# Kernel tuning notes

Hardware: AMD Instinct MI355X
Metric: run time of the kernel (lower is better)

Reference implementation:

```python
import jax, jax.numpy as jnp
import numpy as np

HEADS = 8


def _ln(x, g, b):
    m = x.mean(-1, keepdims=True)
    v = ((x - m) ** 2).mean(-1, keepdims=True)
    return (x - m) / jnp.sqrt(v + 1e-5) * g + b


def _mha(xq, xkv, inw, inb, outw, outb):
    # torch nn.MultiheadAttention (dropout off). xq/xkv: [B,S,D]
    B, S, D = xq.shape
    hd = D // HEADS
    q = (xq @ inw[:D].T + inb[:D]).reshape(B, S, HEADS, hd)
    k = (xkv @ inw[D:2 * D].T + inb[D:2 * D]).reshape(B, S, HEADS, hd)
    v = (xkv @ inw[2 * D:].T + inb[2 * D:]).reshape(B, S, HEADS, hd)
    s = jnp.einsum('bqhd,bkhd->bhqk', q, k) / np.float32(np.sqrt(hd))
    o = jnp.einsum('bhqk,bkhd->bqhd', jax.nn.softmax(s, axis=-1), v).reshape(B, S, D)
    return o @ outw.T + outb


def _eca(x1, x2, qw, qb, kw, kb, vw, vb):
    # EfficientCrossAttention: bmm -> clamp -> softmax -> bmm
    Q = x1 @ qw.T + qb
    K = x2 @ kw.T + kb
    V = x2 @ vw.T + vb
    s = jnp.einsum('bqd,bkd->bqk', Q, K) / np.float32(np.sqrt(Q.shape[-1]))
    s = jnp.clip(s, -100.0, 100.0)
    return jnp.einsum('bqk,bkd->bqd', jax.nn.softmax(s, axis=-1), V)


def _itda(img, caps, qw, qb, kw, kb, vw, vb):
    B, NC, D = caps.shape
    S = img.shape[1]  # 196
    cap_e = jnp.broadcast_to(caps[:, :, None, :], (B, NC, S, D)).reshape(B * NC, S, D)
    img_e = jnp.broadcast_to(img[:, None, :, :], (B, NC, S, D)).reshape(B * NC, S, D)
    out = _eca(cap_e, img_e, qw, qb, kw, kb, vw, vb).reshape(B, NC, S, D)
    mask = (caps.sum(-1) != 0).astype(out.dtype)[:, :, None, None]  # [B,NC,1,1]
    msum = jnp.clip(jnp.broadcast_to(mask, (B, NC, S, 1)).sum(1), 1e-6, None)
    return (out * mask).sum(1) / msum


def _mse(a, b):
    return jnp.mean((a - b) ** 2)


def _forward(input_1, input_2, cap1, cap2, img_w, img_b, w_emb, h_emb,
             mlp_w1, mlp_b1, mlp_w2, mlp_b2, fc_w, fc_b, efc_w, efc_b,
             efc2_w, efc2_b, tr_in_w, tr_in_b, tr_out_w, tr_out_b,
             tr_ln_g, tr_ln_b, itda_qw, itda_qb, itda_kw, itda_kb, itda_vw, itda_vb,
             ca_qw, ca_qb, ca_kw, ca_kb, ca_vw, ca_vb,
             sa_qw, sa_qb, sa_kw, sa_kb, sa_vw, sa_vb):
    B, C, H, W = input_1.shape
    A = img_w.shape[0]
    # caption projections
    cap1_o = cap1 @ fc_w.T + fc_b  # [B,NC,512]
    cap2_o = cap2 @ fc_w.T + fc_b
    cap1_m = jnp.broadcast_to(cap1_o.mean(1)[:, None, :], (B, H * W, A))
    cap2_m = jnp.broadcast_to(cap2_o.mean(1)[:, None, :], (B, H * W, A))
    # 1x1 conv + positional embedding; pe[i,j] = [w_emb[j], h_emb[i]]
    pe = jnp.concatenate([jnp.broadcast_to(w_emb[None, :, :], (W, W, A // 2)),
                          jnp.broadcast_to(h_emb[:, None, :], (H, H, A // 2))], axis=-1)

    def embed(x):
        y = jnp.einsum('bchw,ac->bhwa', x, img_w) + img_b + pe
        return y.reshape(B, H * W, A)

    x1 = embed(input_1)  # [B,196,512]
    x2 = embed(input_2)
    # CDCR (Barlow-Twins style) loss

    def mlp(x):
        return jax.nn.relu(x @ mlp_w1.T + mlp_b1) @ mlp_w2.T + mlp_b2

    f1 = mlp(x1.reshape(-1, A))
    f2 = mlp(x2.reshape(-1, A))
    z_a = (f1 - f1.mean(0)) / jnp.std(f1, axis=0, ddof=1)
    z_b = (f2 - f2.mean(0)) / jnp.std(f2, axis=0, ddof=1)
    Bt, D = z_a.shape
    c = (z_a.T @ z_b) / Bt
    on_diag = jnp.sum((jnp.diagonal(c) - 1.0) ** 2)
    off_diag = jnp.sum(c.reshape(-1)[1:].reshape(D - 1, D + 1)[:, :-1] ** 2)
    cdcr_loss = on_diag + 0.003 * off_diag
    # cross-transformer stack (simultaneous update, as in torch tuple RHS)
    h1, h2 = x1, x2
    for l in range(tr_in_w.shape[0]):
        def layer(q, kv):
            a = _mha(q, kv, tr_in_w[l], tr_in_b[l], tr_out_w[l], tr_out_b[l])
            return _ln(q + a, tr_ln_g[l], tr_ln_b[l])
        h1, h2 = layer(h1, h2), layer(h2, h1)
    diff1 = x1 - h1
    diff2 = x2 - h2
    # ITDA module
    c12 = _eca(diff1, diff2, ca_qw, ca_qb, ca_kw, ca_kb, ca_vw, ca_vb)
    c21 = _eca(diff2, diff1, ca_qw, ca_qb, ca_kw, ca_kb, ca_vw, ca_vb)
    s11 = _eca(diff1, diff1, sa_qw, sa_qb, sa_kw, sa_kb, sa_vw, sa_vb)
    s22 = _eca(diff2, diff2, sa_qw, sa_qb, sa_kw, sa_kb, sa_vw, sa_vb)
    d_bef = _itda(diff1, cap2_o, itda_qw, itda_qb, itda_kw, itda_kb, itda_vw, itda_vb)
    d_aft = _itda(diff2, cap1_o, itda_qw, itda_qb, itda_kw, itda_kb, itda_vw, itda_vb)
    s_bef = _itda(diff1, cap1_o, itda_qw, itda_qb, itda_kw, itda_kb, itda_vw, itda_vb)
    s_aft = _itda(diff2, cap2_o, itda_qw, itda_qb, itda_kw, itda_kb, itda_vw, itda_vb)
    img_to_txt_loss = _mse(d_bef, c12) + _mse(d_aft, c21) + _mse(s_bef, s11) + _mse(s_aft, s22)

    def efc(x):
        return jax.nn.relu(x @ efc_w.T + efc_b)

    dyn = efc(jnp.concatenate([d_bef, d_aft], -1))
    sta = efc(jnp.concatenate([s_bef, s_aft], -1))
    align = efc(jnp.concatenate([dyn, sta], -1))
    txt = efc(jnp.concatenate([cap1_m, cap2_m], -1))
    comb = jnp.concatenate([diff1, diff2, txt, align], -1)  # [B,196,2048]
    out = jax.nn.relu(comb @ efc2_w.T + efc2_b)
    return out, cdcr_loss, img_to_txt_loss


def setup_inputs() -> dict:
    key = jax.random.key(0)
    ks = iter(jax.random.split(key, 64))

    def nrm(shape, s=0.02):
        return jax.random.normal(next(ks), shape, jnp.float32) * s

    B, C, H, W, NC, A = 64, 1024, 14, 14, 16, 512
    inp = dict(
        input_1=jax.random.normal(next(ks), (B, C, H, W), jnp.float32),
        input_2=jax.random.normal(next(ks), (B, C, H, W), jnp.float32),
        cap1=jax.random.normal(next(ks), (B, NC, 768), jnp.float32),
        cap2=jax.random.normal(next(ks), (B, NC, 768), jnp.float32),
        img_w=nrm((A, C)), img_b=jnp.zeros((A,), jnp.float32),
        w_emb=nrm((14, A // 2)), h_emb=nrm((14, A // 2)),
        mlp_w1=nrm((4 * A, A)), mlp_b1=jnp.zeros((4 * A,), jnp.float32),
        mlp_w2=nrm((A, 4 * A)), mlp_b2=jnp.zeros((A,), jnp.float32),
        fc_w=nrm((A, 768)), fc_b=jnp.zeros((A,), jnp.float32),
        efc_w=nrm((A, 2 * A)), efc_b=jnp.zeros((A,), jnp.float32),
        efc2_w=nrm((A, 4 * A)), efc2_b=jnp.zeros((A,), jnp.float32),
        tr_in_w=nrm((2, 3 * A, A)), tr_in_b=jnp.zeros((2, 3 * A), jnp.float32),
        tr_out_w=nrm((2, A, A)), tr_out_b=jnp.zeros((2, A), jnp.float32),
        tr_ln_g=jnp.ones((2, A), jnp.float32), tr_ln_b=jnp.zeros((2, A), jnp.float32),
    )
    for pfx in ('itda', 'ca', 'sa'):
        for nm in ('q', 'k', 'v'):
            inp[pfx + '_' + nm + 'w'] = nrm((A, A))
            inp[pfx + '_' + nm + 'b'] = jnp.zeros((A,), jnp.float32)
    return inp


def reference(input_1, input_2, cap1, cap2, img_w, img_b, w_emb, h_emb,
              mlp_w1, mlp_b1, mlp_w2, mlp_b2, fc_w, fc_b, efc_w, efc_b,
              efc2_w, efc2_b, tr_in_w, tr_in_b, tr_out_w, tr_out_b,
              tr_ln_g, tr_ln_b, itda_qw, itda_qb, itda_kw, itda_kb, itda_vw, itda_vb,
              ca_qw, ca_qb, ca_kw, ca_kb, ca_vw, ca_vb,
              sa_qw, sa_qb, sa_kw, sa_kb, sa_vw, sa_vb):
    return _forward(input_1, input_2, cap1, cap2, img_w, img_b, w_emb, h_emb,
                    mlp_w1, mlp_b1, mlp_w2, mlp_b2, fc_w, fc_b, efc_w, efc_b,
                    efc2_w, efc2_b, tr_in_w, tr_in_b, tr_out_w, tr_out_b,
                    tr_ln_g, tr_ln_b, itda_qw, itda_qb, itda_kw, itda_kb, itda_vw, itda_vb,
                    ca_qw, ca_qb, ca_kw, ca_kb, ca_vw, ca_vb,
                    sa_qw, sa_qb, sa_kw, sa_kb, sa_vw, sa_vb)
```

## Files before the change

kernel.cpp:

```cpp
#include <hip/hip_runtime.h>
#include <hip/hip_bf16.h>
#include <stdint.h>
#include <math.h>

#define BB   64
#define SS   196
#define BS   12544
#define NOUT 6422528L
#define SLD  224

typedef __attribute__((ext_vector_type(8))) short bf16x8;
typedef __attribute__((ext_vector_type(4))) float f32x4;

__device__ __forceinline__ float block_red256(float v, float* red, bool ismax) {
#pragma unroll
  for (int o = 32; o > 0; o >>= 1) {
    float t = __shfl_down(v, o, 64);
    v = ismax ? fmaxf(v, t) : v + t;
  }
  int lane = threadIdx.x & 63, wid = threadIdx.x >> 6;
  if (lane == 0) red[wid] = v;
  __syncthreads();
  float r = ismax ? fmaxf(fmaxf(red[0], red[1]), fmaxf(red[2], red[3]))
                  : (red[0] + red[1]) + (red[2] + red[3]);
// ... 18 lines not shown
__device__ __forceinline__ void lds_barrier() {
  asm volatile("s_waitcnt lgkmcnt(0)" ::: "memory");
  __builtin_amdgcn_s_barrier();
  __builtin_amdgcn_sched_barrier(0);
}

__device__ __forceinline__ int xcd_swizzle(int flat, int nwg) {
  int q = nwg >> 3, r = nwg & 7;
  int xcd = flat & 7, pos = flat >> 3;
  return (xcd < r ? xcd * (q + 1) : r * (q + 1) + (xcd - r) * q) + pos;
}

__global__ __launch_bounds__(256) void k_mfma_nt(
    const float* __restrict__ A, const float* __restrict__ W,
    const float* __restrict__ bias, float* __restrict__ C,
    int M, int N, int K, int relu) {
  __shared__ short As[2][128][40];
  __shared__ short Bs[2][128][40];
  const int tid = threadIdx.x;
  const int lane = tid & 63, wave = tid >> 6;
  const int wm = wave >> 1, wn = wave & 1;
  const int NX = gridDim.x;
  const int wg = xcd_swizzle(blockIdx.y * NX + blockIdx.x, NX * gridDim.y);
  const int m0 = (wg / NX) * 128, n0 = (wg % NX) * 128;
  const int srow = tid >> 1, skh = (tid & 1) * 16;
  const float* Ap = A + (long)(m0 + srow) * K + skh;
  const float* Wp = W + (long)(n0 + srow) * K + skh;
  const int fr = lane & 15, fq = lane >> 4;
  const int NK = K >> 5;
  f32x4 acc[4][4] = {};
  float4 xa[4], xw[4], ya[4], yw[4];
// ... 27 lines not shown
    for (int i = 0; i < 4; ++i)
#pragma unroll
      for (int j = 0; j < 4; ++j)
        acc[i][j] = __builtin_amdgcn_mfma_f32_16x16x32_bf16(af[i], bfr[j], acc[i][j], 0, 0, 0);
    lds_barrier();
  };

  ldt(xa, xw, 0);
  stage(xa, xw, 0);
  if (NK > 1) ldt(xa, xw, 1);
  lds_barrier();
  int t = 0;
  for (; t + 1 < NK; t += 2) { step(t, ya, yw, xa, xw); step(t + 1, xa, xw, ya, yw); }
  if (t < NK) step(t, ya, yw, xa, xw);

#pragma unroll
  for (int i = 0; i < 4; ++i) {
    int mB = m0 + wm * 64 + i * 16 + fq * 4;
#pragma unroll
    for (int j = 0; j < 4; ++j) {
      int n = n0 + wn * 64 + j * 16 + fr;
      float bz = bias[n];
#pragma unroll
      for (int r2 = 0; r2 < 4; ++r2) {
        float v = acc[i][j][r2] + bz;
        if (relu) v = fmaxf(v, 0.f);
        C[(long)(mB + r2) * N + n] = v;
      }
    }
  }
}

__global__ __launch_bounds__(256) void k_mfma_embed(
    const float* __restrict__ X1, const float* __restrict__ X2,
    const float* __restrict__ W,
    const float* __restrict__ bias,
    const float* __restrict__ wemb, const float* __restrict__ hemb,
    const float* __restrict__ sub1, const float* __restrict__ sub2,
    float* __restrict__ C1, float* __restrict__ C2,
    float* __restrict__ D1, float* __restrict__ D2) {
  __shared__ short As[2][128][40];
  __shared__ short Bs[2][128][40];
  const float* X = blockIdx.z ? X2 : X1;
  const float* sub = blockIdx.z ? sub2 : sub1;
  float* C = blockIdx.z ? C2 : C1;
  float* D = blockIdx.z ? D2 : D1;
  const int tid = threadIdx.x;
  const int lane = tid & 63, wave = tid >> 6;
  const int wm = wave >> 1, wn = wave & 1;
  const int NX = gridDim.x;
  const int wg = xcd_swizzle(blockIdx.y * NX + blockIdx.x, NX * gridDim.y);
  const int m0 = (wg / NX) * 128, n0 = (wg % NX) * 128;
  const int K = 1024, N = 512;
  const int srow = tid >> 1, skh = (tid & 1) * 16;
  const float* Wp = W + (long)(n0 + srow) * K + skh;
  const int arow = tid & 127, khalf = tid >> 7;
  const int am = m0 + arow;
  const int ab = am / 196, as_ = am % 196;
  const float* Xp = X + (long)ab * 200704 + as_;
  const int fr = lane & 15, fq = lane >> 4;
  const int NK = K >> 5;
// ... 44 lines not shown
  for (; t + 1 < NK; t += 2) { step(t, yx, yw, xx, xw); step(t + 1, xx, xw, yx, yw); }
  if (t < NK) step(t, yx, yw, xx, xw);

#pragma unroll
  for (int i = 0; i < 4; ++i) {
    int mB = m0 + wm * 64 + i * 16 + fq * 4;
#pragma unroll
    for (int j = 0; j < 4; ++j) {
      int n = n0 + wn * 64 + j * 16 + fr;
      float bz = bias[n];
#pragma unroll
      for (int r2 = 0; r2 < 4; ++r2) {
        int m = mB + r2;
        int s = m % 196;
        float pe = (n < 256) ? wemb[(s % 14) * 256 + n] : hemb[(s / 14) * 256 + (n - 256)];
        float v = acc[i][j][r2] + bz + pe;
        if (sub) v -= sub[(long)m * N + n];
        C[(long)m * N + n] = v;
        if (D) D[(long)m * N + n] = v;
      }
    }
  }
}

__global__ __launch_bounds__(256) void k_fmha(
    const float* __restrict__ Q, const float* __restrict__ KV,
    float* __restrict__ O) {
  __shared__ short Vt[64][240];
  __shared__ short Pt[4][16][40];
  const int tid = threadIdx.x;
  const int lane = tid & 63, wave = tid >> 6;
  const int b = blockIdx.x, h = blockIdx.y;
  const long brow = (long)b * 196;
  const float* Qb = Q + brow * 512 + h * 64;
  const float* Kb = KV + brow * 1024 + h * 64;
  const float* Vb = KV + brow * 1024 + 512 + h * 64;
  float* Ob = O + brow * 512 + h * 64;
  const int fr = lane & 15, fq = lane >> 4;

  for (int i = tid; i < 64 * 32; i += 256) {
    int d = i >> 5, k = 192 + (i & 31);
    if (k >= 196) Vt[d][k] = 0;
  }
  for (int i = tid; i < 196 * 16; i += 256) {
    int s = i >> 4, c4 = (i & 15) * 4;
    float4 v = *(const float4*)(Vb + (long)s * 1024 + c4);
    Vt[c4 + 0][s] = f2bf(v.x);
    Vt[c4 + 1][s] = f2bf(v.y);
    Vt[c4 + 2][s] = f2bf(v.z);
    Vt[c4 + 3][s] = f2bf(v.w);
  }
  __syncthreads();

  for (int qt = wave; qt < 13; qt += 4) {
    const int q0 = qt * 16;
    const int qr = (q0 + fr < 196) ? q0 + fr : 195;
    bf16x8 aq0, aq1;
    {
      const float* qp = Qb + (long)qr * 512 + fq * 8;
      float4 a = *(const float4*)(qp);
      float4 b2 = *(const float4*)(qp + 4);
      float4 c = *(const float4*)(qp + 32);
      float4 d = *(const float4*)(qp + 36);
      cvt8((short*)&aq0, a, b2);
      cvt8((short*)&aq1, c, d);
    }
    f32x4 sc[13];
#pragma unroll
    for (int t = 0; t < 13; ++t) {
      int kr = (t * 16 + fr < 196) ? t * 16 + fr : 195;
      const float* kp = Kb + (long)kr * 1024 + fq * 8;
      float4 a = *(const float4*)(kp);
      float4 b2 = *(const float4*)(kp + 4);
      float4 c = *(const float4*)(kp + 32);
      float4 d = *(const float4*)(kp + 36);
      bf16x8 bk0, bk1;
      cvt8((short*)&bk0, a, b2);
      cvt8((short*)&bk1, c, d);
      f32x4 z = {};
      z = __builtin_amdgcn_mfma_f32_16x16x32_bf16(aq0, bk0, z, 0, 0, 0);
      z = __builtin_amdgcn_mfma_f32_16x16x32_bf16(aq1, bk1, z, 0, 0, 0);
      sc[t] = z;
    }
#pragma unroll
    for (int t = 0; t < 13; ++t)
#pragma unroll
      for (int r2 = 0; r2 < 4; ++r2) sc[t][r2] *= 0.125f;
    if (fr >= 4) {
#pragma unroll
      for (int r2 = 0; r2 < 4; ++r2) sc[12][r2] = -1e30f;
    }
#pragma unroll
    for (int r2 = 0; r2 < 4; ++r2) {
// ... 109 lines not shown
      int mb = m0 + i * 16 + fq * 4;
#pragma unroll
      for (int r2 = 0; r2 < 4; ++r2) {
        int m = mb + r2;
        if (m < M) {
          float v = acc[i][r2] * scale + bz;
          if (relu2) v = fmaxf(v, 0.f);
          if (clampf) v = fminf(fmaxf(v, -100.f), 100.f);
          Cb[(long)m * ldc + n] = v;
        }
      }
    }
  }
}

__global__ __launch_bounds__(256) void k_mfma_bnn(
    const float* __restrict__ A, const float* __restrict__ B, float* __restrict__ C,
    int M, int N, int K, int KBvalid, int lda, int ldb, int ldc, int nz2,
    int64_t sA1, int64_t sA2, int64_t sB1, int64_t sB2, int64_t sC1, int64_t sC2) {
  __shared__ short As[2][64][40];
  __shared__ short Bs[2][64][40];
  const int tid = threadIdx.x;
  const int lane = tid & 63, wave = tid >> 6;
  const int m0 = blockIdx.y * 64, n0 = blockIdx.x * 64;
  const int z = blockIdx.z, z1 = z / nz2, z2 = z % nz2;
  const float* Ab = A + z1 * sA1 + z2 * sA2;
  const float* Bb = B + z1 * sB1 + z2 * sB2;
  float* Cb = C + z1 * sC1 + z2 * sC2;
  const int sr = tid >> 2, skh = (tid & 3) * 8;
  const int ar = (m0 + sr < M) ? m0 + sr : M - 1;
// ... 109 lines not shown
  lds_barrier();
  int t = 0;
  for (; t + 1 < NK; t += 2) { step(t, ya, yb, xa, xb); step(t + 1, xa, xb, ya, yb); }
  if (t < NK) step(t, ya, yb, xa, xb);

  const int j = j0 + wave * 16 + fr;
#pragma unroll
  for (int i = 0; i < 4; ++i) {
    int ib = i0 + i * 16 + fq * 4;
#pragma unroll
    for (int r2 = 0; r2 < 4; ++r2)
      atomicAdd(&C[(long)(ib + r2) * 512 + j], acc[i][r2] * scale);
  }
}

__global__ __launch_bounds__(256) void k_gemm_nt(
    const float* __restrict__ A, const float* __restrict__ W,
    const float* __restrict__ bias, float* __restrict__ C,
    int M, int N, int K, int relu) {
  __shared__ float As[16][68];
  __shared__ float Ws[16][68];
  const int tx = threadIdx.x, ty = threadIdx.y;
  const int tid = ty * 16 + tx;
  const int m0 = blockIdx.y * 64, n0 = blockIdx.x * 64;
  const int lr = tid >> 2, lk = (tid & 3) << 2;
  const float* Ap = A + (long)(m0 + lr) * K + lk;
  const float* Wp = W + (long)(n0 + lr) * K + lk;
  float acc[4][4] = {};
  for (int k0 = 0; k0 < K; k0 += 16) {
    float4 av = *(const float4*)(Ap + k0);
    float4 wv = *(const float4*)(Wp + k0);
    As[lk + 0][lr] = av.x; As[lk + 1][lr] = av.y; As[lk + 2][lr] = av.z; As[lk + 3][lr] = av.w;
    Ws[lk + 0][lr] = wv.x; Ws[lk + 1][lr] = wv.y; Ws[lk + 2][lr] = wv.z; Ws[lk + 3][lr] = wv.w;
    __syncthreads();
#pragma unroll
    for (int kk = 0; kk < 16; ++kk) {
      float4 a4 = *(const float4*)&As[kk][ty * 4];
      float4 w4 = *(const float4*)&Ws[kk][tx * 4];
      float a[4] = {a4.x, a4.y, a4.z, a4.w};
      float w[4] = {w4.x, w4.y, w4.z, w4.w};
#pragma unroll
      for (int i = 0; i < 4; ++i)
#pragma unroll
        for (int j = 0; j < 4; ++j) acc[i][j] += a[i] * w[j];
    }
    __syncthreads();
  }
#pragma unroll
  for (int i = 0; i < 4; ++i) {
    int m = m0 + ty * 4 + i;
#pragma unroll
    for (int j = 0; j < 4; ++j) {
      int n = n0 + tx * 4 + j;
      float v = acc[i][j] + bias[n];
      if (relu) v = fmaxf(v, 0.f);
      C[(long)m * N + n] = v;
    }
  }
}

__global__ __launch_bounds__(256) void k_softmax_rows(float* __restrict__ S, int nrows) {
  int row = blockIdx.x * 4 + (threadIdx.x >> 6);
  int lane = threadIdx.x & 63;
  if (row >= nrows) return;
  float* p = S + (long)row * SLD;
  float v0 = p[lane];
  float v1 = p[lane + 64];
  float v2 = p[lane + 128];
  float v3 = (lane + 192 < 196) ? p[lane + 192] : -1e30f;
  float mx = fmaxf(fmaxf(v0, v1), fmaxf(v2, v3));
#pragma unroll
  for (int o = 32; o > 0; o >>= 1) mx = fmaxf(mx, __shfl_down(mx, o, 64));
  mx = __shfl(mx, 0, 64);
  float e0 = expf(v0 - mx), e1 = expf(v1 - mx), e2 = expf(v2 - mx);
  float e3 = (lane + 192 < 196) ? expf(v3 - mx) : 0.f;
  float s = e0 + e1 + e2 + e3;
#pragma unroll
  for (int o = 32; o > 0; o >>= 1) s += __shfl_down(s, o, 64);
  s = __shfl(s, 0, 64);
  float inv = 1.0f / s;
  p[lane] = e0 * inv;
  p[lane + 64] = e1 * inv;
  p[lane + 128] = e2 * inv;
  if (lane + 192 < SLD) p[lane + 192] = (lane + 192 < 196) ? e3 * inv : 0.f;
}

__global__ __launch_bounds__(256) void k_addln(
    float* __restrict__ h, const float* __restrict__ o,
    const float* __restrict__ g, const float* __restrict__ be) {
  __shared__ float red[4];
  long row = blockIdx.x;
  float* hr = h + row * 512;
  const float* orow = o + row * 512;
  int t = threadIdx.x;
  float v0 = hr[t] + orow[t];
  float v1 = hr[t + 256] + orow[t + 256];
  float mean = block_red256(v0 + v1, red, false) * (1.0f / 512.0f);
  float d0 = v0 - mean, d1 = v1 - mean;
  float var = block_red256(d0 * d0 + d1 * d1, red, false) * (1.0f / 512.0f);
  float inv = 1.0f / sqrtf(var + 1e-5f);
  hr[t] = d0 * inv * g[t] + be[t];
  hr[t + 256] = d1 * inv * g[t + 256] + be[t + 256];
}

__global__ void k_zero(float* __restrict__ p, int n) {
  int i = blockIdx.x * 256 + threadIdx.x;
  if (i < n) p[i] = 0.f;
}

__global__ __launch_bounds__(256) void k_diff(
    float* __restrict__ d, const float* __restrict__ x, const float* __restrict__ h) {
  long i = ((long)blockIdx.x * 256 + threadIdx.x) * 4;
  float4 xv = *(const float4*)(x + i);
  float4 hv = *(const float4*)(h + i);
  float4 r; r.x = xv.x - hv.x; r.y = xv.y - hv.y; r.z = xv.z - hv.z; r.w = xv.w - hv.w;
  *(float4*)(d + i) = r;
}
// ... 125 lines not shown
  __syncthreads();
  for (int st = 128; st > 0; st >>= 1) {
    if (threadIdx.x < st) sh[threadIdx.x] += sh[threadIdx.x + st];
    __syncthreads();
  }
  if (threadIdx.x == 0) out[0] = (float)(sh[0] / (64.0 * 196.0 * 512.0));
}

__global__ __launch_bounds__(256) void k_concat2(float* __restrict__ dst, const float* __restrict__ a,
                                                 const float* __restrict__ b) {
  int i = blockIdx.x * 256 + threadIdx.x;
  int col = i & 1023, row = i >> 10;
  dst[i] = (col < 512) ? a[row * 512 + col] : b[row * 512 + col - 512];
}

__global__ __launch_bounds__(256) void k_comb_chunk(
    float* __restrict__ dst, const float* __restrict__ d1, const float* __restrict__ d2,
    const float* __restrict__ txt, const float* __restrict__ al, long r0) {
  long i = (long)blockIdx.x * 256 + threadIdx.x;
  int col = (int)(i & 2047);
  long m = r0 + (i >> 11);
  int b = (int)(m / 196);
  float v;
  if (col < 512)       v = d1[m * 512 + col];
  else if (col < 1024) v = d2[m * 512 + col - 512];
  else if (col < 1536) v = txt[(long)b * 512 + col - 1024];
  else                 v = al[(long)b * 512 + col - 1536];
  dst[i] = v;
}

extern "C" void kernel_launch(void* const* d_in, const int* in_sizes, int n_in,
                              void* d_out, int out_size, void* d_ws, size_t ws_size,
                              hipStream_t stream) {
  (void)in_sizes; (void)n_in; (void)out_size;
  const float* in1    = (const float*)d_in[0];
  const float* in2    = (const float*)d_in[1];
  const float* cap1   = (const float*)d_in[2];
  const float* cap2   = (const float*)d_in[3];
  const float* imgw   = (const float*)d_in[4];
  const float* imgb   = (const float*)d_in[5];
  const float* wemb   = (const float*)d_in[6];
  const float* hemb   = (const float*)d_in[7];
  const float* mlpw1  = (const float*)d_in[8];
  const float* mlpb1  = (const float*)d_in[9];
  const float* mlpw2  = (const float*)d_in[10];
  const float* mlpb2  = (const float*)d_in[11];
  const float* fcw    = (const float*)d_in[12];
  const float* fcb    = (const float*)d_in[13];
  const float* efcw   = (const float*)d_in[14];
// ... 21 lines not shown
  const size_t SZ = (size_t)BS * 512;
  float* w = (float*)d_ws;
  auto alloc = [&](size_t n) { float* p = w; w += n; return p; };
  float* h1 = alloc(SZ);
  float* h2 = alloc(SZ);
  float* tA = alloc(SZ);
  float* tB = alloc(SZ);
  float* tC = alloc(SZ);
  float* tD = alloc(SZ);
  float* sbuf = alloc(SZ);
  float* cap1o = alloc(64 * 16 * 512);
  float* cap2o = alloc(64 * 16 * 512);
  float* qc1   = alloc(64 * 16 * 512);
  float* qc2   = alloc(64 * 16 * 512);
  float* attb  = alloc(64 * 16 * 512);
  float* cmat  = alloc(512 * 512);
  float* colsum1 = alloc(512); float* colsq1 = alloc(512);
  float* colsum2 = alloc(512); float* colsq2 = alloc(512);
  float* mean1 = alloc(512); float* istd1 = alloc(512);
  float* mean2 = alloc(512); float* istd2 = alloc(512);
  float* mask1 = alloc(1024); float* mask2 = alloc(1024);
  float* vdbef = alloc(64 * 512); float* vdaft = alloc(64 * 512);
  float* vsbef = alloc(64 * 512); float* vsaft = alloc(64 * 512);
  float* cm1 = alloc(64 * 512); float* cm2 = alloc(64 * 512);
  float* vdyn = alloc(64 * 512); float* vsta = alloc(64 * 512);
  float* valign = alloc(64 * 512); float* vtxt = alloc(64 * 512);
  float* ccat = alloc(64 * 1024);
  double* msepart = (double*)alloc(4096 * 2);
  double* cdcrpart = (double*)alloc(1024);
  float* itkvw = alloc(1024 * 512); float* itkvb = alloc(1024);
  float* cakvw = alloc(1024 * 512); float* cakvb = alloc(1024);
  float* sakvw = alloc(1024 * 512); float* sakvb = alloc(1024);
  size_t used = (size_t)(w - (float*)d_ws);
  bool xsave = ws_size >= (used + 2 * SZ + 1024) * sizeof(float);
  float* x1 = nullptr;
  if (xsave) x1 = alloc(2 * SZ);

  auto gemm = [&](const float* Aa, const float* Ww, const float* bb, float* Cc,
                  int M, int N, int K, int relu) {
    long g128 = ((M % 128) == 0 && (N % 128) == 0) ? (long)(N / 128) * (M / 128) : 0;
    if (g128 >= 784 && (K % 32) == 0)
      k_mfma_nt<<<dim3(N / 128, M / 128), 256, 0, stream>>>(Aa, Ww, bb, Cc, M, N, K, relu);
    else
      k_mfma_bnt<<<dim3(N / 64, (M + 63) / 64, 1), 256, 0, stream>>>(
          Aa, Ww, Cc, M, N, K, K, K, N, 1,
          0, 0, 0, 0, 0, 0, 1.0f, 0, bb, relu);
  };
  auto embed2 = [&](const float* s1, const float* s2, float* C1p, float* C2p,
                    float* D1p, float* D2p) {
    k_mfma_embed<<<dim3(4, BS / 128, 2), 256, 0, stream>>>(
        in1, in2, imgw, imgb, wemb, hemb, s1, s2, C1p, C2p, D1p, D2p);
  };
  const int64_t RB = (int64_t)SS * 512;
  const int64_t QB = 16 * 512;
  auto attn512 = [&](const float* Qp, int64_t qZ, const float* KVp, int64_t kvZ,
                     float* Op, int64_t oZ, int M, float scale) {
    int mt = (M + 63) / 64;
    int64_t sS = (int64_t)M * SLD;
    k_mfma_bnt<<<dim3(4, mt, 64), 256, 0, stream>>>(
        Qp, KVp, sbuf, M, 196, 512, 512, 1024, SLD, 1,
        qZ, 0, kvZ, 0, sS, 0, scale, 1, nullptr, 0);
    k_softmax_rows<<<(64 * M + 3) / 4, 256, 0, stream>>>(sbuf, 64 * M);
    k_mfma_bnn<<<dim3(8, mt, 64), 256, 0, stream>>>(
        sbuf, KVp + 512, Op, M, 512, SLD, 196, SLD, 1024, 512, 1,
        sS, 0, kvZ, 0, oZ, 0);
  };
  auto attn_mha = [&](const float* Qp, const float* KVp, float* Op) {
    k_fmha<<<dim3(64, 8), 256, 0, stream>>>(Qp, KVp, Op);
  };
  auto efc64 = [&](const float* Aa, float* Cc) {
    k_mfma_bnt<<<dim3(8, 1, 1), 256, 0, stream>>>(
        Aa, efcw, Cc, 64, 512, 1024, 1024, 1024, 512, 1,
        0, 0, 0, 0, 0, 0, 1.0f, 0, efcb, 1);
  };

  const float scalE = 1.0f / sqrtf(512.0f);

  k_catkv<<<2048, 256, 0, stream>>>(itkvw, itkw, itvw, itkvb, itkb, itvb);
  k_catkv<<<2048, 256, 0, stream>>>(cakvw, cakw, cavw, cakvb, cakb, cavb);
  k_catkv<<<2048, 256, 0, stream>>>(sakvw, sakw, savw, sakvb, sakb, savb);

  if (xsave) embed2(nullptr, nullptr, h1, h2, x1, x1 + SZ);
  else       embed2(nullptr, nullptr, h1, h2, nullptr, nullptr);
  gemm(cap1, fcw, fcb, cap1o, 1024, 512, 768, 0);
  gemm(cap2, fcw, fcb, cap2o, 1024, 512, 768, 0);
  k_meannc<<<dim3(2, 64), 256, 0, stream>>>(cap1o, nullptr, cm1);
  k_meannc<<<dim3(2, 64), 256, 0, stream>>>(cap2o, nullptr, cm2);

  for (int c = 0; c < 2; ++c) {
    const size_t off = (size_t)c * 6272 * 512;
    gemm(h1 + off, mlpw1, mlpb1, tC, 6272, 2048, 512, 1);
    gemm(tC, mlpw2, mlpb2, tA + off, 6272, 512, 2048, 0);
  }
  for (int c = 0; c < 2; ++c) {
    const size_t off = (size_t)c * 6272 * 512;
    gemm(h2 + off, mlpw1, mlpb1, tC, 6272, 2048, 512, 1);
    gemm(tC, mlpw2, mlpb2, tB + off, 6272, 512, 2048, 0);
  }
  k_zero<<<8, 256, 0, stream>>>(colsum1, 2048);
  k_colstats<<<dim3(16, 49), 256, 0, stream>>>(tA, colsum1, colsq1);
  k_colstats<<<dim3(16, 49), 256, 0, stream>>>(tB, colsum2, colsq2);
  k_finstats<<<2, 256, 0, stream>>>(colsum1, colsq1, mean1, istd1);
  k_finstats<<<2, 256, 0, stream>>>(colsum2, colsq2, mean2, istd2);
  k_znorm<<<25088, 256, 0, stream>>>(tA, mean1, istd1);
  k_znorm<<<25088, 256, 0, stream>>>(tB, mean2, istd2);
  k_zero<<<1024, 256, 0, stream>>>(cmat, 262144);
  k_mfma_corr<<<dim3(8, 8, 14), 256, 0, stream>>>(tA, tB, cmat, BS / 14, 1.0f / (float)BS);
  k_cdcr_part<<<256, 256, 0, stream>>>(cmat, cdcrpart);
  k_cdcr_fin<<<1, 256, 0, stream>>>(cdcrpart, out + NOUT);

  for (int l = 0; l < 2; ++l) {
    const float* Wq = trinw + (size_t)l * 1536 * 512;
    const float* Wkv = Wq + 512 * 512;
    const float* bq = trinb + l * 1536;
    const float* bkv = bq + 512;
    const float* Wo = troutw + (size_t)l * 512 * 512;
    const float* bo = troutb + l * 512;
    const float* g  = trlng + l * 512;
    const float* be = trlnb + l * 512;
    gemm(h1, Wq, bq, tA, 2 * BS, 512, 512, 0);
    gemm(h2, Wkv, bkv, tC, BS, 1024, 512, 0);
    attn_mha(tA, tC, tA);
    gemm(tA, Wo, bo, sbuf, BS, 512, 512, 0);
    gemm(h1, Wkv, bkv, tC, BS, 1024, 512, 0);
    k_addln<<<BS, 256, 0, stream>>>(h1, sbuf, g, be);
    attn_mha(tA + SZ, tC, tA + SZ);
    gemm(tA + SZ, Wo, bo, sbuf, BS, 512, 512, 0);
    k_addln<<<BS, 256, 0, stream>>>(h2, sbuf, g, be);
  }

  if (xsave) {
    k_diff<<<12544, 256, 0, stream>>>(tC, x1, h1);
  } else {
    embed2(h1, h2, tC, tD, nullptr, nullptr);
  }

  gemm(cap1o, itqw, itqb, qc1, 1024, 512, 512, 0);
  gemm(cap2o, itqw, itqb, qc2, 1024, 512, 512, 0);
  k_mask<<<1024, 64, 0, stream>>>(cap1o, mask1);
  k_mask<<<1024, 64, 0, stream>>>(cap2o, mask2);
  gemm(tC, itkvw, itkvb, tA, BS, 1024, 512, 0);
  attn512(qc2, QB, tA, 2 * RB, attb, QB, 16, scalE);
  k_meannc<<<dim3(2, 64), 256, 0, stream>>>(attb, mask2, vdbef);
  attn512(qc1, QB, tA, 2 * RB, attb, QB, 16, scalE);
  k_meannc<<<dim3(2, 64), 256, 0, stream>>>(attb, mask1, vsbef);
  gemm(tD, itkvw, itkvb, tA, BS, 1024, 512, 0);
  attn512(qc1, QB, tA, 2 * RB, attb, QB, 16, scalE);
  k_meannc<<<dim3(2, 64), 256, 0, stream>>>(attb, mask1, vdaft);
  attn512(qc2, QB, tA, 2 * RB, attb, QB, 16, scalE);
  k_meannc<<<dim3(2, 64), 256, 0, stream>>>(attb, mask2, vsaft);

  auto eca_mse = [&](const float* xq, const float* xkv,
                     const float* qw2, const float* qb2,
                     const float* kvw2, const float* kvb2,
                     const float* vec, double* part) {
    gemm(xq,  qw2, qb2, h1, BS, 512, 512, 0);
    gemm(xkv, kvw2, kvb2, tA, BS, 1024, 512, 0);
    attn512(h1, RB, tA, 2 * RB, h2, RB, 196, scalE);
    k_mse<<<1024, 256, 0, stream>>>(h2, vec, part);
  };
  eca_mse(tC, tD, caqw, caqb, cakvw, cakvb, vdbef, msepart);
  eca_mse(tD, tC, caqw, caqb, cakvw, cakvb, vdaft, msepart + 1024);
  eca_mse(tC, tC, saqw, saqb, sakvw, sakvb, vsbef, msepart + 2048);
  eca_mse(tD, tD, saqw, saqb, sakvw, sakvb, vsaft, msepart + 3072);
  k_finloss<<<1, 256, 0, stream>>>(msepart, out + NOUT + 1);

  k_concat2<<<256, 256, 0, stream>>>(ccat, vdbef, vdaft);
  efc64(ccat, vdyn);
  k_concat2<<<256, 256, 0, stream>>>(ccat, vsbef, vsaft);
  efc64(ccat, vsta);
  k_concat2<<<256, 256, 0, stream>>>(ccat, vdyn, vsta);
  efc64(ccat, valign);
  k_concat2<<<256, 256, 0, stream>>>(ccat, cm1, cm2);
  efc64(ccat, vtxt);

  k_comb_chunk<<<100352, 256, 0, stream>>>(h1, tC, tD, vtxt, valign, 0);
  gemm(h1, efc2w, efc2b, out, BS, 512, 2048, 1);
}
```

Baseline: 2.544 ms.

## Store GEMM intermediates as bf16, batch attention calls, drop fallback embed path

GEMM outputs that only feed later MFMA stages (MLP hidden, transformer Q/KV, the concat before the final FC) are now written as bf16. A new GEMM variant reads bf16 A operands, and the fused MHA kernel reads bf16 Q/K/V directly, which cuts memory traffic and conversion work. The MLP runs over the full batch instead of in chunks, and paired ITDA attention calls are batched through a second z dimension. The embedding is stored once instead of being written to several buffers, and the xsave fallback is removed. In exchange this adds bf16 rounding to intermediates and assumes the workspace is large enough, and it uses qc1/qc2 and attb/attb2 as if they were contiguous.

```diff
diff --git a/kernel.cpp b/kernel.cpp
--- a/kernel.cpp
+++ b/kernel.cpp
@@ -56,7 +56,7 @@
 __global__ __launch_bounds__(256) void k_mfma_nt(
     const float* __restrict__ A, const float* __restrict__ W,
     const float* __restrict__ bias, float* __restrict__ C,
-    int M, int N, int K, int relu) {
+    int M, int N, int K, int relu, int obf) {
   __shared__ short As[2][128][40];
   __shared__ short Bs[2][128][40];
   const int tid = threadIdx.x;
@@ -114,6 +114,7 @@
   for (; t + 1 < NK; t += 2) { step(t, ya, yw, xa, xw); step(t + 1, xa, xw, ya, yw); }
   if (t < NK) step(t, ya, yw, xa, xw);
 
+  short* Cs = (short*)C;
 #pragma unroll
   for (int i = 0; i < 4; ++i) {
     int mB = m0 + wm * 64 + i * 16 + fq * 4;
@@ -125,7 +126,8 @@
       for (int r2 = 0; r2 < 4; ++r2) {
         float v = acc[i][j][r2] + bz;
         if (relu) v = fmaxf(v, 0.f);
-        C[(long)(mB + r2) * N + n] = v;
+        if (obf) Cs[(long)(mB + r2) * N + n] = f2bf(v);
+        else     C[(long)(mB + r2) * N + n] = v;
       }
     }
   }
@@ -136,15 +138,11 @@
     const float* __restrict__ W,
     const float* __restrict__ bias,
     const float* __restrict__ wemb, const float* __restrict__ hemb,
-    const float* __restrict__ sub1, const float* __restrict__ sub2,
-    float* __restrict__ C1, float* __restrict__ C2,
-    float* __restrict__ D1, float* __restrict__ D2) {
+    float* __restrict__ C1, float* __restrict__ C2) {
   __shared__ short As[2][128][40];
   __shared__ short Bs[2][128][40];
   const float* X = blockIdx.z ? X2 : X1;
-  const float* sub = blockIdx.z ? sub2 : sub1;
   float* C = blockIdx.z ? C2 : C1;
-  float* D = blockIdx.z ? D2 : D1;
   const int tid = threadIdx.x;
   const int lane = tid & 63, wave = tid >> 6;
   const int wm = wave >> 1, wn = wave & 1;
@@ -219,17 +217,14 @@
         int m = mB + r2;
         int s = m % 196;
         float pe = (n < 256) ? wemb[(s % 14) * 256 + n] : hemb[(s / 14) * 256 + (n - 256)];
-        float v = acc[i][j][r2] + bz + pe;
-        if (sub) v -= sub[(long)m * N + n];
-        C[(long)m * N + n] = v;
-        if (D) D[(long)m * N + n] = v;
+        C[(long)m * N + n] = acc[i][j][r2] + bz + pe;
       }
     }
   }
 }
 
-__global__ __launch_bounds__(256) void k_fmha(
-    const float* __restrict__ Q, const float* __restrict__ KV,
+__global__ __launch_bounds__(256) void k_fmha_bf(
+    const short* __restrict__ Q, const short* __restrict__ KV,
     float* __restrict__ O) {
   __shared__ short Vt[64][240];
   __shared__ short Pt[4][16][40];
@@ -237,9 +232,9 @@
   const int lane = tid & 63, wave = tid >> 6;
   const int b = blockIdx.x, h = blockIdx.y;
   const long brow = (long)b * 196;
-  const float* Qb = Q + brow * 512 + h * 64;
-  const float* Kb = KV + brow * 1024 + h * 64;
-  const float* Vb = KV + brow * 1024 + 512 + h * 64;
+  const short* Qb = Q + brow * 512 + h * 64;
+  const short* Kb = KV + brow * 1024 + h * 64;
+  const short* Vb = KV + brow * 1024 + 512 + h * 64;
   float* Ob = O + brow * 512 + h * 64;
   const int fr = lane & 15, fq = lane >> 4;
 
@@ -247,41 +242,27 @@
     int d = i >> 5, k = 192 + (i & 31);
     if (k >= 196) Vt[d][k] = 0;
   }
-  for (int i = tid; i < 196 * 16; i += 256) {
-    int s = i >> 4, c4 = (i & 15) * 4;
-    float4 v = *(const float4*)(Vb + (long)s * 1024 + c4);
-    Vt[c4 + 0][s] = f2bf(v.x);
-    Vt[c4 + 1][s] = f2bf(v.y);
-    Vt[c4 + 2][s] = f2bf(v.z);
-    Vt[c4 + 3][s] = f2bf(v.w);
+  for (int i = tid; i < 196 * 8; i += 256) {
+    int s = i >> 3, c8 = (i & 7) * 8;
+    bf16x8 v = *(const bf16x8*)(Vb + (long)s * 1024 + c8);
+#pragma unroll
+    for (int j = 0; j < 8; ++j) Vt[c8 + j][s] = v[j];
   }
   __syncthreads();
 
   for (int qt = wave; qt < 13; qt += 4) {
     const int q0 = qt * 16;
     const int qr = (q0 + fr < 196) ? q0 + fr : 195;
-    bf16x8 aq0, aq1;
-    {
-      const float* qp = Qb + (long)qr * 512 + fq * 8;
-      float4 a = *(const float4*)(qp);
-      float4 b2 = *(const float4*)(qp + 4);
-      float4 c = *(const float4*)(qp + 32);
-      float4 d = *(const float4*)(qp + 36);
-      cvt8((short*)&aq0, a, b2);
-      cvt8((short*)&aq1, c, d);
-    }
+    const short* qp = Qb + (long)qr * 512 + fq * 8;
+    bf16x8 aq0 = *(const bf16x8*)(qp);
+    bf16x8 aq1 = *(const bf16x8*)(qp + 32);
     f32x4 sc[13];
 #pragma unroll
     for (int t = 0; t < 13; ++t) {
       int kr = (t * 16 + fr < 196) ? t * 16 + fr : 195;
-      const float* kp = Kb + (long)kr * 1024 + fq * 8;
-      float4 a = *(const float4*)(kp);
-      float4 b2 = *(const float4*)(kp + 4);
-      float4 c = *(const float4*)(kp + 32);
-      float4 d = *(const float4*)(kp + 36);
-      bf16x8 bk0, bk1;
-      cvt8((short*)&bk0, a, b2);
-      cvt8((short*)&bk1, c, d);
+      const short* kp = Kb + (long)kr * 1024 + fq * 8;
+      bf16x8 bk0 = *(const bf16x8*)(kp);
+      bf16x8 bk1 = *(const bf16x8*)(kp + 32);
       f32x4 z = {};
       z = __builtin_amdgcn_mfma_f32_16x16x32_bf16(aq0, bk0, z, 0, 0, 0);
       z = __builtin_amdgcn_mfma_f32_16x16x32_bf16(aq1, bk1, z, 0, 0, 0);
@@ -421,6 +402,79 @@
   }
 }
 
+__global__ __launch_bounds__(256) void k_mfma_bnt_abf(
+    const short* __restrict__ A, const float* __restrict__ B, float* __restrict__ C,
+    int M, int N, int K, int lda, int ldb, int ldc,
+    const float* __restrict__ bias2, int relu2) {
+  __shared__ short As[2][64][40];
+  __shared__ short Bs[2][64][40];
+  const int tid = threadIdx.x;
+  const int lane = tid & 63, wave = tid >> 6;
+  const int NX = gridDim.x;
+  const int wg = xcd_swizzle(blockIdx.y * NX + blockIdx.x, NX * gridDim.y);
+  const int m0 = (wg / NX) * 64, n0 = (wg % NX) * 64;
+  const int sr = tid >> 2, skh = (tid & 3) * 8;
+  const int ar = (m0 + sr < M) ? m0 + sr : M - 1;
+  const int br = (n0 + sr < N) ? n0 + sr : N - 1;
+  const short* Ap = A + (long)ar * lda + skh;
+  const float* Bp = B + (long)br * ldb + skh;
+  const int fr = lane & 15, fq = lane >> 4;
+  const int NK = K >> 5;
+  f32x4 acc[4] = {};
+  int4 xa, ya;
+  float4 xb[2], yb[2];
+
+  auto ldt = [&](int4& ta, float4 (&tb)[2], int t) {
+    const int kb = t * 32;
+    ta = *(const int4*)(Ap + kb);
+#pragma unroll
+    for (int i = 0; i < 2; ++i) tb[i] = *(const float4*)(Bp + kb + i * 4);
+  };
+  auto stage = [&](int4& ta, float4 (&tb)[2], int p) {
+    *(int4*)&As[p][sr][skh] = ta;
+    cvt8(&Bs[p][sr][skh], tb[0], tb[1]);
+  };
+  auto step = [&](int t, int4& la, float4 (&lb)[2], int4& ca, float4 (&cb)[2]) {
+    const int par = t & 1;
+    if (t + 2 < NK) ldt(la, lb, t + 2);
+    bf16x8 bfr = *(const bf16x8*)&Bs[par][wave * 16 + fr][fq * 8];
+    bf16x8 af[4];
+#pragma unroll
+    for (int i = 0; i < 4; ++i) af[i] = *(const bf16x8*)&As[par][i * 16 + fr][fq * 8];
+    if (t + 1 < NK) stage(ca, cb, par ^ 1);
+#pragma unroll
+    for (int i = 0; i < 4; ++i)
+      acc[i] = __builtin_amdgcn_mfma_f32_16x16x32_bf16(af[i], bfr, acc[i], 0, 0, 0);
+    lds_barrier();
+  };
+
+  ldt(xa, xb, 0);
+  stage(xa, xb, 0);
+  if (NK > 1) ldt(xa, xb, 1);
+  lds_barrier();
+  int t = 0;
+  for (; t + 1 < NK; t += 2) { step(t, ya, yb, xa, xb); step(t + 1, xa, xb, ya, yb); }
+  if (t < NK) step(t, ya, yb, xa, xb);
+
+  const int n = n0 + wave * 16 + fr;
+  if (n < N) {
+    float bz = bias2 ? bias2[n] : 0.f;
+#pragma unroll
+    for (int i = 0; i < 4; ++i) {
+      int mb = m0 + i * 16 + fq * 4;
+#pragma unroll
+      for (int r2 = 0; r2 < 4; ++r2) {
+        int m = mb + r2;
+        if (m < M) {
+          float v = acc[i][r2] + bz;
+          if (relu2) v = fmaxf(v, 0.f);
+          C[(long)m * ldc + n] = v;
+        }
+      }
+    }
+  }
+}
+
 __global__ __launch_bounds__(256) void k_mfma_bnn(
     const float* __restrict__ A, const float* __restrict__ B, float* __restrict__ C,
     int M, int N, int K, int KBvalid, int lda, int ldb, int ldc, int nz2,
@@ -560,51 +614,6 @@
   }
 }
 
-__global__ __launch_bounds__(256) void k_gemm_nt(
-    const float* __restrict__ A, const float* __restrict__ W,
-    const float* __restrict__ bias, float* __restrict__ C,
-    int M, int N, int K, int relu) {
-  __shared__ float As[16][68];
-  __shared__ float Ws[16][68];
-  const int tx = threadIdx.x, ty = threadIdx.y;
-  const int tid = ty * 16 + tx;
-  const int m0 = blockIdx.y * 64, n0 = blockIdx.x * 64;
-  const int lr = tid >> 2, lk = (tid & 3) << 2;
-  const float* Ap = A + (long)(m0 + lr) * K + lk;
-  const float* Wp = W + (long)(n0 + lr) * K + lk;
-  float acc[4][4] = {};
-  for (int k0 = 0; k0 < K; k0 += 16) {
-    float4 av = *(const float4*)(Ap + k0);
-    float4 wv = *(const float4*)(Wp + k0);
-    As[lk + 0][lr] = av.x; As[lk + 1][lr] = av.y; As[lk + 2][lr] = av.z; As[lk + 3][lr] = av.w;
-    Ws[lk + 0][lr] = wv.x; Ws[lk + 1][lr] = wv.y; Ws[lk + 2][lr] = wv.z; Ws[lk + 3][lr] = wv.w;
-    __syncthreads();
-#pragma unroll
-    for (int kk = 0; kk < 16; ++kk) {
-      float4 a4 = *(const float4*)&As[kk][ty * 4];
-      float4 w4 = *(const float4*)&Ws[kk][tx * 4];
-      float a[4] = {a4.x, a4.y, a4.z, a4.w};
-      float w[4] = {w4.x, w4.y, w4.z, w4.w};
-#pragma unroll
-      for (int i = 0; i < 4; ++i)
-#pragma unroll
-        for (int j = 0; j < 4; ++j) acc[i][j] += a[i] * w[j];
-    }
-    __syncthreads();
-  }
-#pragma unroll
-  for (int i = 0; i < 4; ++i) {
-    int m = m0 + ty * 4 + i;
-#pragma unroll
-    for (int j = 0; j < 4; ++j) {
-      int n = n0 + tx * 4 + j;
-      float v = acc[i][j] + bias[n];
-      if (relu) v = fmaxf(v, 0.f);
-      C[(long)m * N + n] = v;
-    }
-  }
-}
-
 __global__ __launch_bounds__(256) void k_softmax_rows(float* __restrict__ S, int nrows) {
   int row = blockIdx.x * 4 + (threadIdx.x >> 6);
   int lane = threadIdx.x & 63;
@@ -631,22 +640,23 @@
   if (lane + 192 < SLD) p[lane + 192] = (lane + 192 < 196) ? e3 * inv : 0.f;
 }
 
-__global__ __launch_bounds__(256) void k_addln(
-    float* __restrict__ h, const float* __restrict__ o,
+__global__ __launch_bounds__(256) void k_addln2(
+    float* __restrict__ dst, const float* __restrict__ src, const float* __restrict__ o,
     const float* __restrict__ g, const float* __restrict__ be) {
   __shared__ float red[4];
   long row = blockIdx.x;
-  float* hr = h + row * 512;
+  const float* sr_ = src + row * 512;
   const float* orow = o + row * 512;
+  float* dr = dst + row * 512;
   int t = threadIdx.x;
-  float v0 = hr[t] + orow[t];
-  float v1 = hr[t + 256] + orow[t + 256];
+  float v0 = sr_[t] + orow[t];
+  float v1 = sr_[t + 256] + orow[t + 256];
   float mean = block_red256(v0 + v1, red, false) * (1.0f / 512.0f);
   float d0 = v0 - mean, d1 = v1 - mean;
   float var = block_red256(d0 * d0 + d1 * d1, red, false) * (1.0f / 512.0f);
   float inv = 1.0f / sqrtf(var + 1e-5f);
-  hr[t] = d0 * inv * g[t] + be[t];
-  hr[t + 256] = d1 * inv * g[t + 256] + be[t + 256];
+  dr[t] = d0 * inv * g[t] + be[t];
+  dr[t + 256] = d1 * inv * g[t + 256] + be[t + 256];
 }
 
 __global__ void k_zero(float* __restrict__ p, int n) {
@@ -802,25 +812,25 @@
   dst[i] = (col < 512) ? a[row * 512 + col] : b[row * 512 + col - 512];
 }
 
-__global__ __launch_bounds__(256) void k_comb_chunk(
-    float* __restrict__ dst, const float* __restrict__ d1, const float* __restrict__ d2,
-    const float* __restrict__ txt, const float* __restrict__ al, long r0) {
+__global__ __launch_bounds__(256) void k_comb_bf(
+    short* __restrict__ dst, const float* __restrict__ d1, const float* __restrict__ d2,
+    const float* __restrict__ txt, const float* __restrict__ al) {
   long i = (long)blockIdx.x * 256 + threadIdx.x;
   int col = (int)(i & 2047);
-  long m = r0 + (i >> 11);
+  long m = i >> 11;
   int b = (int)(m / 196);
   float v;
   if (col < 512)       v = d1[m * 512 + col];
   else if (col < 1024) v = d2[m * 512 + col - 512];
   else if (col < 1536) v = txt[(long)b * 512 + col - 1024];
   else                 v = al[(long)b * 512 + col - 1536];
-  dst[i] = v;
+  dst[i] = f2bf(v);
 }
 
 extern "C" void kernel_launch(void* const* d_in, const int* in_sizes, int n_in,
                               void* d_out, int out_size, void* d_ws, size_t ws_size,
                               hipStream_t stream) {
-  (void)in_sizes; (void)n_in; (void)out_size;
+  (void)in_sizes; (void)n_in; (void)out_size; (void)ws_size;
   const float* in1    = (const float*)d_in[0];
   const float* in2    = (const float*)d_in[1];
   const float* cap1   = (const float*)d_in[2];
@@ -872,6 +882,7 @@
   float* qc1   = alloc(64 * 16 * 512);
   float* qc2   = alloc(64 * 16 * 512);
   float* attb  = alloc(64 * 16 * 512);
+  float* attb2 = alloc(64 * 16 * 512);
   float* cmat  = alloc(512 * 512);
   float* colsum1 = alloc(512); float* colsq1 = alloc(512);
   float* colsum2 = alloc(512); float* colsq2 = alloc(512);
@@ -889,42 +900,36 @@
   float* itkvw = alloc(1024 * 512); float* itkvb = alloc(1024);
   float* cakvw = alloc(1024 * 512); float* cakvb = alloc(1024);
   float* sakvw = alloc(1024 * 512); float* sakvb = alloc(1024);
-  size_t used = (size_t)(w - (float*)d_ws);
-  bool xsave = ws_size >= (used + 2 * SZ + 1024) * sizeof(float);
-  float* x1 = nullptr;
-  if (xsave) x1 = alloc(2 * SZ);
+  float* x1 = alloc(2 * SZ);
+  float* x2 = x1 + SZ;
 
   auto gemm = [&](const float* Aa, const float* Ww, const float* bb, float* Cc,
                   int M, int N, int K, int relu) {
     long g128 = ((M % 128) == 0 && (N % 128) == 0) ? (long)(N / 128) * (M / 128) : 0;
     if (g128 >= 784 && (K % 32) == 0)
-      k_mfma_nt<<<dim3(N / 128, M / 128), 256, 0, stream>>>(Aa, Ww, bb, Cc, M, N, K, relu);
+      k_mfma_nt<<<dim3(N / 128, M / 128), 256, 0, stream>>>(Aa, Ww, bb, Cc, M, N, K, relu, 0);
     else
       k_mfma_bnt<<<dim3(N / 64, (M + 63) / 64, 1), 256, 0, stream>>>(
           Aa, Ww, Cc, M, N, K, K, K, N, 1,
           0, 0, 0, 0, 0, 0, 1.0f, 0, bb, relu);
   };
-  auto embed2 = [&](const float* s1, const float* s2, float* C1p, float* C2p,
-                    float* D1p, float* D2p) {
-    k_mfma_embed<<<dim3(4, BS / 128, 2), 256, 0, stream>>>(
-        in1, in2, imgw, imgb, wemb, hemb, s1, s2, C1p, C2p, D1p, D2p);
-  };
   const int64_t RB = (int64_t)SS * 512;
   const int64_t QB = 16 * 512;
-  auto attn512 = [&](const float* Qp, int64_t qZ, const float* KVp, int64_t kvZ,
-                     float* Op, int64_t oZ, int M, float scale) {
+  auto attn512 = [&](const float* Qp, int64_t qZ1, int64_t qZ2, const float* KVp, int64_t kvZ,
+                     float* Op, int64_t oZ1, int64_t oZ2, int M, int zq, float scale) {
     int mt = (M + 63) / 64;
-    int64_t sS = (int64_t)M * SLD;
-    k_mfma_bnt<<<dim3(4, mt, 64), 256, 0, stream>>>(
-        Qp, KVp, sbuf, M, 196, 512, 512, 1024, SLD, 1,
-        qZ, 0, kvZ, 0, sS, 0, scale, 1, nullptr, 0);
-    k_softmax_rows<<<(64 * M + 3) / 4, 256, 0, stream>>>(sbuf, 64 * M);
-    k_mfma_bnn<<<dim3(8, mt, 64), 256, 0, stream>>>(
-        sbuf, KVp + 512, Op, M, 512, SLD, 196, SLD, 1024, 512, 1,
-        sS, 0, kvZ, 0, oZ, 0);
-  };
-  auto attn_mha = [&](const float* Qp, const float* KVp, float* Op) {
-    k_fmha<<<dim3(64, 8), 256, 0, stream>>>(Qp, KVp, Op);
+    int64_t sS2 = (int64_t)M * SLD;
+    int64_t sS1 = 64 * sS2;
+    k_mfma_bnt<<<dim3(4, mt, 64 * zq), 256, 0, stream>>>(
+        Qp, KVp, sbuf, M, 196, 512, 512, 1024, SLD, 64,
+        qZ1, qZ2, 0, kvZ, sS1, sS2, scale, 1, nullptr, 0);
+    k_softmax_rows<<<(64 * zq * M + 3) / 4, 256, 0, stream>>>(sbuf, 64 * zq * M);
+    k_mfma_bnn<<<dim3(8, mt, 64 * zq), 256, 0, stream>>>(
+        sbuf, KVp + 512, Op, M, 512, SLD, 196, SLD, 1024, 512, 64,
+        sS1, sS2, 0, kvZ, oZ1, oZ2);
+  };
+  auto attn_mha = [&](const short* Qp, const short* KVp, float* Op) {
+    k_fmha_bf<<<dim3(64, 8), 256, 0, stream>>>(Qp, KVp, Op);
   };
   auto efc64 = [&](const float* Aa, float* Cc) {
     k_mfma_bnt<<<dim3(8, 1, 1), 256, 0, stream>>>(
@@ -938,23 +943,19 @@
   k_catkv<<<2048, 256, 0, stream>>>(cakvw, cakw, cavw, cakvb, cakb, cavb);
   k_catkv<<<2048, 256, 0, stream>>>(sakvw, sakw, savw, sakvb, sakb, savb);
 
-  if (xsave) embed2(nullptr, nullptr, h1, h2, x1, x1 + SZ);
-  else       embed2(nullptr, nullptr, h1, h2, nullptr, nullptr);
+  k_mfma_embed<<<dim3(4, BS / 128, 2), 256, 0, stream>>>(
+      in1, in2, imgw, imgb, wemb, hemb, x1, x2);
   gemm(cap1, fcw, fcb, cap1o, 1024, 512, 768, 0);
   gemm(cap2, fcw, fcb, cap2o, 1024, 512, 768, 0);
   k_meannc<<<dim3(2, 64), 256, 0, stream>>>(cap1o, nullptr, cm1);
   k_meannc<<<dim3(2, 64), 256, 0, stream>>>(cap2o, nullptr, cm2);
 
-  for (int c = 0; c < 2; ++c) {
-    const size_t off = (size_t)c * 6272 * 512;
-    gemm(h1 + off, mlpw1, mlpb1, tC, 6272, 2048, 512, 1);
-    gemm(tC, mlpw2, mlpb2, tA + off, 6272, 512, 2048, 0);
-  }
-  for (int c = 0; c < 2; ++c) {
-    const size_t off = (size_t)c * 6272 * 512;
-    gemm(h2 + off, mlpw1, mlpb1, tC, 6272, 2048, 512, 1);
-    gemm(tC, mlpw2, mlpb2, tB + off, 6272, 512, 2048, 0);
-  }
+  k_mfma_nt<<<dim3(16, 98), 256, 0, stream>>>(x1, mlpw1, mlpb1, tC, BS, 2048, 512, 1, 1);
+  k_mfma_bnt_abf<<<dim3(8, 196), 256, 0, stream>>>(
+      (const short*)tC, mlpw2, tA, BS, 512, 2048, 2048, 2048, 512, mlpb2, 0);
+  k_mfma_nt<<<dim3(16, 98), 256, 0, stream>>>(x2, mlpw1, mlpb1, tC, BS, 2048, 512, 1, 1);
+  k_mfma_bnt_abf<<<dim3(8, 196), 256, 0, stream>>>(
+      (const short*)tC, mlpw2, tB, BS, 512, 2048, 2048, 2048, 512, mlpb2, 0);
   k_zero<<<8, 256, 0, stream>>>(colsum1, 2048);
   k_colstats<<<dim3(16, 49), 256, 0, stream>>>(tA, colsum1, colsq1);
   k_colstats<<<dim3(16, 49), 256, 0, stream>>>(tB, colsum2, colsq2);
@@ -976,37 +977,34 @@
     const float* bo = troutb + l * 512;
     const float* g  = trlng + l * 512;
     const float* be = trlnb + l * 512;
-    gemm(h1, Wq, bq, tA, 2 * BS, 512, 512, 0);
-    gemm(h2, Wkv, bkv, tC, BS, 1024, 512, 0);
-    attn_mha(tA, tC, tA);
-    gemm(tA, Wo, bo, sbuf, BS, 512, 512, 0);
-    gemm(h1, Wkv, bkv, tC, BS, 1024, 512, 0);
-    k_addln<<<BS, 256, 0, stream>>>(h1, sbuf, g, be);
-    attn_mha(tA + SZ, tC, tA + SZ);
-    gemm(tA + SZ, Wo, bo, sbuf, BS, 512, 512, 0);
-    k_addln<<<BS, 256, 0, stream>>>(h2, sbuf, g, be);
-  }
-
-  if (xsave) {
-    k_diff<<<12544, 256, 0, stream>>>(tC, x1, h1);
-  } else {
-    embed2(h1, h2, tC, tD, nullptr, nullptr);
-  }
-
-  gemm(cap1o, itqw, itqb, qc1, 1024, 512, 512, 0);
-  gemm(cap2o, itqw, itqb, qc2, 1024, 512, 512, 0);
+    const float* s1 = l ? h1 : x1;
+    const float* s2 = l ? h2 : x2;
+    k_mfma_nt<<<dim3(4, 196), 256, 0, stream>>>(s1, Wq, bq, tA, 2 * BS, 512, 512, 0, 1);
+    k_mfma_nt<<<dim3(8, 98), 256, 0, stream>>>(s2, Wkv, bkv, tC, BS, 1024, 512, 0, 1);
+    k_mfma_nt<<<dim3(8, 98), 256, 0, stream>>>(s1, Wkv, bkv, tD, BS, 1024, 512, 0, 1);
+    attn_mha((const short*)tA, (const short*)tC, tB);
+    k_mfma_bnt<<<dim3(8, 196, 1), 256, 0, stream>>>(tB, Wo, sbuf, BS, 512, 512, 512, 512, 512, 1,
+                                                    0, 0, 0, 0, 0, 0, 1.0f, 0, bo, 0);
+    k_addln2<<<BS, 256, 0, stream>>>(h1, s1, sbuf, g, be);
+    attn_mha((const short*)tA + (size_t)BS * 512, (const short*)tD, tB);
+    k_mfma_bnt<<<dim3(8, 196, 1), 256, 0, stream>>>(tB, Wo, sbuf, BS, 512, 512, 512, 512, 512, 1,
+                                                    0, 0, 0, 0, 0, 0, 1.0f, 0, bo, 0);
+    k_addln2<<<BS, 256, 0, stream>>>(h2, s2, sbuf, g, be);
+  }
+
+  k_diff<<<12544, 256, 0, stream>>>(tC, x1, h1);
+
+  gemm(cap1o, itqw, itqb, qc1, 2048, 512, 512, 0);
   k_mask<<<1024, 64, 0, stream>>>(cap1o, mask1);
   k_mask<<<1024, 64, 0, stream>>>(cap2o, mask2);
   gemm(tC, itkvw, itkvb, tA, BS, 1024, 512, 0);
-  attn512(qc2, QB, tA, 2 * RB, attb, QB, 16, scalE);
-  k_meannc<<<dim3(2, 64), 256, 0, stream>>>(attb, mask2, vdbef);
-  attn512(qc1, QB, tA, 2 * RB, attb, QB, 16, scalE);
-  k_meannc<<<dim3(2, 64), 256, 0, stream>>>(attb, mask1, vsbef);
+  attn512(qc1, 524288, QB, tA, 2 * RB, attb, 524288, QB, 16, 2, scalE);
+  k_meannc<<<dim3(2, 64), 256, 0, stream>>>(attb,  mask1, vsbef);
+  k_meannc<<<dim3(2, 64), 256, 0, stream>>>(attb2, mask2, vdbef);
   gemm(tD, itkvw, itkvb, tA, BS, 1024, 512, 0);
-  attn512(qc1, QB, tA, 2 * RB, attb, QB, 16, scalE);
-  k_meannc<<<dim3(2, 64), 256, 0, stream>>>(attb, mask1, vdaft);
-  attn512(qc2, QB, tA, 2 * RB, attb, QB, 16, scalE);
-  k_meannc<<<dim3(2, 64), 256, 0, stream>>>(attb, mask2, vsaft);
+  attn512(qc1, 524288, QB, tA, 2 * RB, attb, 524288, QB, 16, 2, scalE);
+  k_meannc<<<dim3(2, 64), 256, 0, stream>>>(attb,  mask1, vdaft);
+  k_meannc<<<dim3(2, 64), 256, 0, stream>>>(attb2, mask2, vsaft);
 
   auto eca_mse = [&](const float* xq, const float* xkv,
                      const float* qw2, const float* qb2,
@@ -1014,7 +1012,7 @@
                      const float* vec, double* part) {
     gemm(xq,  qw2, qb2, h1, BS, 512, 512, 0);
     gemm(xkv, kvw2, kvb2, tA, BS, 1024, 512, 0);
-    attn512(h1, RB, tA, 2 * RB, h2, RB, 196, scalE);
+    attn512(h1, 0, RB, tA, 2 * RB, h2, 0, RB, 196, 1, scalE);
     k_mse<<<1024, 256, 0, stream>>>(h2, vec, part);
   };
   eca_mse(tC, tD, caqw, caqb, cakvw, cakvb, vdbef, msepart);
@@ -1032,6 +1030,7 @@
   k_concat2<<<256, 256, 0, stream>>>(ccat, cm1, cm2);
   efc64(ccat, vtxt);
 
-  k_comb_chunk<<<100352, 256, 0, stream>>>(h1, tC, tD, vtxt, valign, 0);
-  gemm(h1, efc2w, efc2b, out, BS, 512, 2048, 1);
-}
+  k_comb_bf<<<100352, 256, 0, stream>>>((short*)h1, tC, tD, vtxt, valign);
+  k_mfma_bnt_abf<<<dim3(8, 196), 256, 0, stream>>>(
+      (const short*)h1, efc2w, out, BS, 512, 2048, 2048, 2048, 512, efc2b, 1);
+}
```

Result: faster. 2.383 ms (-6.3%).
